# Kernel tuning notes

Hardware: AMD Instinct MI355X
Metric: run time of the kernel (lower is better)

## Reference

```python
import jax, jax.numpy as jnp
import numpy as np
from jax import lax

Tx, Ty, NA, NS = 30, 10, 32, 64
HV, MV = 128, 64
B = 16384


def setup_inputs() -> dict:
    key = jax.random.key(0)
    ks = jax.random.split(key, 16)
    g = lambda k, s: jax.random.normal(k, s, jnp.float32) * 0.05
    return {
        "X": jax.random.normal(ks[0], (B, Tx, HV), jnp.float32),
        # pre-attention bidirectional LSTM (PyTorch gate order i,f,g,o; b = b_ih + b_hh)
        "W_ih_f": g(ks[1], (4 * NA, HV)), "W_hh_f": g(ks[2], (4 * NA, NA)), "b_f": g(ks[3], (4 * NA,)),
        "W_ih_r": g(ks[4], (4 * NA, HV)), "W_hh_r": g(ks[5], (4 * NA, NA)), "b_r": g(ks[6], (4 * NA,)),
        # attention MLP
        "W1": g(ks[7], (10, 2 * NA + NS)), "b1": g(ks[8], (10,)),
        "W2": g(ks[9], (1, 10)), "b2": g(ks[10], (1,)),
        # post-attention LSTM cell
        "W_ih_p": g(ks[11], (4 * NS, 2 * NA)), "W_hh_p": g(ks[12], (4 * NS, NS)), "b_p": g(ks[13], (4 * NS,)),
        # output projection
        "Wo": g(ks[14], (MV, NS)), "bo": g(ks[15], (MV,)),
    }


def _cell(x, h, c, W_ih, W_hh, b):
    # PyTorch LSTM cell, gate order (i, f, g, o)
    z = x @ W_ih.T + h @ W_hh.T + b
    i, f, gg, o = jnp.split(z, 4, axis=-1)
    c = jax.nn.sigmoid(f) * c + jax.nn.sigmoid(i) * jnp.tanh(gg)
    h = jax.nn.sigmoid(o) * jnp.tanh(c)
    return h, c


def _run_lstm(X, W_ih, W_hh, b):
    Bn = X.shape[0]
    H = W_hh.shape[1]
    init = (jnp.zeros((Bn, H), X.dtype), jnp.zeros((Bn, H), X.dtype))

    def step(carry, x_t):
        h, c = _cell(x_t, carry[0], carry[1], W_ih, W_hh, b)
        return (h, c), h

    _, hs = lax.scan(step, init, jnp.swapaxes(X, 0, 1))  # hs: [Tx, B, H]
    return jnp.swapaxes(hs, 0, 1)


def reference(X, W_ih_f, W_hh_f, b_f, W_ih_r, W_hh_r, b_r, W1, b1, W2, b2,
              W_ih_p, W_hh_p, b_p, Wo, bo):
    # bidirectional encoder: a is [B, Tx, 2*NA]
    a_f = _run_lstm(X, W_ih_f, W_hh_f, b_f)
    a_r = _run_lstm(X[:, ::-1, :], W_ih_r, W_hh_r, b_r)[:, ::-1, :]
    a = jnp.concatenate([a_f, a_r], axis=-1)
    Bn = X.shape[0]

    def dec_step(carry, _):
        s, c = carry
        # one_step_attention
        s_rep = jnp.broadcast_to(s[:, None, :], (Bn, Tx, NS))
        cat = jnp.concatenate([a, s_rep], axis=-1)          # [B, Tx, 2*NA+NS]
        e = jnp.tanh(cat @ W1.T + b1)                        # [B, Tx, 10]
        en = jax.nn.relu(e @ W2.T + b2)                      # [B, Tx, 1]
        alphas = jax.nn.softmax(en, axis=1)                  # softmax over Tx
        context = jnp.sum(alphas * a, axis=1)                # [B, 2*NA]
        # post-attention LSTM (single step)
        s, c = _cell(context, s, c, W_ih_p, W_hh_p, b_p)
        out = s @ Wo.T + bo                                  # [B, MV]
        return (s, c), out

    init = (jnp.zeros((Bn, NS), X.dtype), jnp.zeros((Bn, NS), X.dtype))
    _, outs = lax.scan(dec_step, init, None, length=Ty)      # [Ty, B, MV]
    return jnp.swapaxes(outs, 0, 1)                          # [B, Ty, MV]
```

## Files before the change

kernel.cpp:

```cpp
#include <hip/hip_runtime.h>

typedef unsigned short u16;
typedef unsigned int   u32;
typedef __attribute__((ext_vector_type(8))) short short8;
typedef __attribute__((ext_vector_type(4))) float f4;

#define BT 16
#define TX 30
#define TY 10

__device__ __forceinline__ float bf2f_u16(u16 h){ u32 i=((u32)h)<<16; float f; __builtin_memcpy(&f,&i,4); return f; }
__device__ __forceinline__ float lo2f(u32 p){ u32 i=p<<16; float f; __builtin_memcpy(&f,&i,4); return f; }
__device__ __forceinline__ float hi2f(u32 p){ u32 i=p&0xffff0000u; float f; __builtin_memcpy(&f,&i,4); return f; }
__device__ __forceinline__ u16 f2bf(float f){ u32 x; __builtin_memcpy(&x,&f,4); u32 r=(x+0x7fffu+((x>>16)&1u))>>16; return (u16)r; }

#if __has_builtin(__builtin_amdgcn_rcpf)
__device__ __forceinline__ float frcp(float x){ return __builtin_amdgcn_rcpf(x); }
#else
__device__ __forceinline__ float frcp(float x){ return 1.0f/x; }
#endif
__device__ __forceinline__ float sigm(float x){ return frcp(1.0f+__expf(-x)); }
__device__ __forceinline__ float tanh_(float x){ x=fminf(fmaxf(x,-15.0f),15.0f); float e=__expf(2.0f*x); return 1.0f - 2.0f*frcp(e+1.0f); }

__device__ __forceinline__ f4 mfma16(short8 a, short8 b, f4 c){
    return __builtin_amdgcn_mfma_f32_16x16x32_bf16(a, b, c, 0, 0, 0);
}

union S8u { short8 s; u32 u[4]; };

__device__ __forceinline__ void cvt_pair(float a0, float a1, u32& hp, u32& lp){
    u32 u0, u1; __builtin_memcpy(&u0,&a0,4); __builtin_memcpy(&u1,&a1,4);
    hp = __builtin_amdgcn_perm(u1, u0, 0x07060302u);
    float r0 = a0 - hi2f(u0);
    float r1 = a1 - hi2f(u1);
    u32 v0, v1; __builtin_memcpy(&v0,&r0,4); __builtin_memcpy(&v1,&r1,4);
    lp = __builtin_amdgcn_perm(v1, v0, 0x07060302u);
}

struct SDec {
    u16 sh[BT][64], sl[BT][64];
    u16 ctxh[BT][64], ctxl[BT][64];
    float en[BT*TX];
};
struct SEnc {
    u16 h[2][2][2][BT][40];
};
union UU { SEnc e; SDec d; };
struct Smem {
    u16 a[BT*TX][64];
    UU u;
};
static_assert(sizeof(SEnc) == 10240, "enc");
static_assert(sizeof(SDec) == 10112, "dec");
static_assert(sizeof(Smem) == 71680, "LDS 70KB -> 2 blocks/CU");

__global__ __launch_bounds__(256, 2) void fused_kernel(
    const float* __restrict__ X,
    const float* __restrict__ Wihf, const float* __restrict__ Whhf, const float* __restrict__ bfv,
    const float* __restrict__ Wihr, const float* __restrict__ Whhr, const float* __restrict__ brv,
    const float* __restrict__ W1, const float* __restrict__ b1, const float* __restrict__ W2, const float* __restrict__ b2,
    const float* __restrict__ Wihp, const float* __restrict__ Whhp, const float* __restrict__ bp,
    const float* __restrict__ Wo, const float* __restrict__ bo,
    float* __restrict__ out)
{
    __shared__ __align__(16) Smem sm;
    const int tid = threadIdx.x;
    const int b0  = blockIdx.x * BT;

    const int lane = tid & 63;
    const int wv   = tid >> 6;
    const int mL   = lane & 15;
    const int qL   = lane >> 4;
    const int k0q  = qL * 8;
    const int ed   = wv >> 1;
    const int ub   = (wv & 1) * 16;

    {
        u32* p = (u32*)&sm.u.e;
        for (int i = tid; i < 2560; i += 256) p[i] = 0u;
    }
    __syncthreads();

    const float* Wih = ed ? Wihr : Wihf;
    const float* Whh = ed ? Whhr : Whhf;
    const float* bv  = ed ? brv  : bfv;

    short8 Bih[4][4]; short8 Bhh[4]; float bias4[4];
    #pragma unroll
    for (int gt = 0; gt < 4; gt++){
        const int n = gt*32 + ub + mL;
        #pragma unroll
        for (int kt = 0; kt < 4; kt++){
            const float* p = Wih + n*128 + kt*32 + k0q;
            short8 s;
            #pragma unroll
            for (int j = 0; j < 8; j++) s[j] = (short)f2bf(p[j]);
            Bih[gt][kt] = s;
        }
        {
            const float* p = Whh + n*32 + k0q;
            short8 s;
            #pragma unroll
            for (int j = 0; j < 8; j++) s[j] = (short)f2bf(p[j]);
            Bhh[gt] = s;
        }
        bias4[gt] = bv[n];
    }

    const float* xrow = X + ((long)(b0 + mL)) * TX * 128;
    float cst[4] = {0.f,0.f,0.f,0.f};

    auto estep = [&](int t, f4* cur, f4* nxt){
        if (t + 1 < TX){
            const int ts = ed ? (TX-2-t) : (t+1);
            const float* p = xrow + ts*128 + k0q;
            #pragma unroll
            for (int kt = 0; kt < 4; kt++){
                nxt[2*kt]   = *(const f4*)(p + kt*32);
                nxt[2*kt+1] = *(const f4*)(p + kt*32 + 4);
            }
        }
        const int rb = (t+1) & 1, wb = t & 1;

        f4 acc[4];
        #pragma unroll
        for (int gt = 0; gt < 4; gt++) acc[gt] = (f4){bias4[gt],bias4[gt],bias4[gt],bias4[gt]};

        #pragma unroll
        for (int kt = 0; kt < 4; kt++){
            S8u xh, xl;
            cvt_pair(cur[2*kt][0],   cur[2*kt][1],   xh.u[0], xl.u[0]);
            cvt_pair(cur[2*kt][2],   cur[2*kt][3],   xh.u[1], xl.u[1]);
            cvt_pair(cur[2*kt+1][0], cur[2*kt+1][1], xh.u[2], xl.u[2]);
            cvt_pair(cur[2*kt+1][2], cur[2*kt+1][3], xh.u[3], xl.u[3]);
            #pragma unroll
            for (int gt = 0; gt < 4; gt++){
                acc[gt] = mfma16(xh.s, Bih[gt][kt], acc[gt]);
                acc[gt] = mfma16(xl.s, Bih[gt][kt], acc[gt]);
            }
        }
        {
            const short8 Ahh = *(const short8*)&sm.u.e.h[rb][ed][0][mL][k0q];
            const short8 Ahl = *(const short8*)&sm.u.e.h[rb][ed][1][mL][k0q];
            #pragma unroll
            for (int gt = 0; gt < 4; gt++){
                acc[gt] = mfma16(Ahh, Bhh[gt], acc[gt]);
                acc[gt] = mfma16(Ahl, Bhh[gt], acc[gt]);
            }
        }
        const int tpos = ed ? (TX-1-t) : t;
        const int u = ed*32 + ub + mL;
        #pragma unroll
        for (int reg = 0; reg < 4; reg++){
            const int m = qL*4 + reg;
            const float ii = sigm(acc[0][reg]), ff = sigm(acc[1][reg]);
            const float gg = tanh_(acc[2][reg]), oo = sigm(acc[3][reg]);
            cst[reg] = ff*cst[reg] + ii*gg;
            const float hh = oo * tanh_(cst[reg]);
            const u16 hhi = f2bf(hh);
            const u16 hlo = f2bf(hh - bf2f_u16(hhi));
            sm.u.e.h[wb][ed][0][m][ub+mL] = hhi;
            sm.u.e.h[wb][ed][1][m][ub+mL] = hlo;
            const int r = m*TX + tpos;
            sm.a[r][(((u>>3) ^ ((m+tpos)&7))<<3) | (u&7)] = hhi;
        }
        __syncthreads();
    };

    f4 rawA[8], rawB[8];
    {
        const int ts0 = ed ? (TX-1) : 0;
        const float* p = xrow + ts0*128 + k0q;
        #pragma unroll
        for (int kt = 0; kt < 4; kt++){
            rawA[2*kt]   = *(const f4*)(p + kt*32);
            rawA[2*kt+1] = *(const f4*)(p + kt*32 + 4);
        }
    }
    for (int t = 0; t < TX; t += 2){ estep(t, rawA, rawB); estep(t+1, rawB, rawA); }

    {
        u32* z = (u32*)sm.u.d.sh;
        for (int i = tid; i < 1024; i += 256) z[i] = 0u;
    }
    short8 W1aB[2][2];
    #pragma unroll
    for (int kt = 0; kt < 2; kt++){
        short8 hv8, lv8;
        #pragma unroll
        for (int j = 0; j < 8; j++){
            const float v = (mL < 10) ? W1[mL*128 + kt*32 + k0q + j] : 0.f;
            const u16 hb = f2bf(v);
            hv8[j] = (short)hb;
            lv8[j] = (short)f2bf(v - bf2f_u16(hb));
        }
        W1aB[kt][0] = hv8; W1aB[kt][1] = lv8;
    }
    short8 W1sB[2];
    #pragma unroll
    for (int kt = 0; kt < 2; kt++){
        short8 s;
        #pragma unroll
        for (int j = 0; j < 8; j++){
            const float v = (mL < 10) ? W1[mL*128 + 64 + kt*32 + k0q + j] : 0.f;
            s[j] = (short)f2bf(v);
        }
        W1sB[kt] = s;
    }
    const float b1v = (mL < 10) ? b1[mL] : 0.f;
    const float w2v = (mL < 10) ? W2[mL] : 0.f;
    const float b2s = b2[0];

    const int uw = wv * 16;
    short8 Bip[4][2], Bhp[4][2]; float pb4[4];
    #pragma unroll
    for (int gt = 0; gt < 4; gt++){
        const int n = gt*64 + uw + mL;
        #pragma unroll
        for (int kt = 0; kt < 2; kt++){
            const float* p = Wihp + n*64 + kt*32 + k0q;
            const float* q = Whhp + n*64 + kt*32 + k0q;
            short8 s1v, s2v;
            #pragma unroll
            for (int j = 0; j < 8; j++){ s1v[j] = (short)f2bf(p[j]); s2v[j] = (short)f2bf(q[j]); }
            Bip[gt][kt] = s1v; Bhp[gt][kt] = s2v;
        }
        pb4[gt] = bp[n];
    }
    short8 Bo2[2];
    {
        const int n = uw + mL;
        #pragma unroll
        for (int kt = 0; kt < 2; kt++){
            const float* p = Wo + n*64 + kt*32 + k0q;
            short8 s;
            #pragma unroll
            for (int j = 0; j < 8; j++) s[j] = (short)f2bf(p[j]);
            Bo2[kt] = s;
        }
    }
    const float boL = bo[uw + mL];
    float cs2[4] = {0.f,0.f,0.f,0.f};
    const u16* aflat  = &sm.a[0][0];
    u16* shf = &sm.u.d.sh[0][0];
    u16* slf = &sm.u.d.sl[0][0];
    u16* chf = &sm.u.d.ctxh[0][0];
    u16* clf = &sm.u.d.ctxl[0][0];
    __syncthreads();

    for (int ty = 0; ty < TY; ty++){
        for (int tt = wv; tt < TX; tt += 4){
            const int r = tt*16 + mL;
            const int b = (r * 34953) >> 20;
            const int tp2 = r - b*30;
            f4 accE = (f4){b1v, b1v, b1v, b1v};
            const u16* ab = aflat + r*64;
            const int keyA = (b + tp2) & 7;
            #pragma unroll
            for (int kt = 0; kt < 2; kt++){
                const short8 av = *(const short8*)(ab + (((kt*4+qL)^keyA)<<3));
                accE = mfma16(av, W1aB[kt][0], accE);
                accE = mfma16(av, W1aB[kt][1], accE);
            }
            const int keyS = b & 7;
            #pragma unroll
            for (int kt = 0; kt < 2; kt++){
                const int off = b*64 + (((kt*4+qL)^keyS)<<3);
                const short8 shh = *(const short8*)(shf + off);
                const short8 sll = *(const short8*)(slf + off);
                accE = mfma16(shh, W1sB[kt], accE);
                accE = mfma16(sll, W1sB[kt], accE);
            }
            float er[4];
            #pragma unroll
            for (int reg = 0; reg < 4; reg++) er[reg] = w2v * tanh_(accE[reg]);
            #pragma unroll
            for (int d = 1; d < 16; d <<= 1){
                #pragma unroll
                for (int reg = 0; reg < 4; reg++) er[reg] += __shfl_xor(er[reg], d);
            }
            if (mL == 0){
                f4 ev;
                #pragma unroll
                for (int reg = 0; reg < 4; reg++) ev[reg] = fmaxf(er[reg] + b2s, 0.f);
                *(f4*)&sm.u.d.en[tt*16 + qL*4] = ev;
            }
        }
        __syncthreads();
        {
            const int cr = tid >> 4, cup = tid & 15;
            const float* enr = &sm.u.d.en[cr*30];
            float mx = enr[0];
            #pragma unroll
            for (int t2 = 1; t2 < TX; t2++) mx = fmaxf(mx, enr[t2]);
            float ssum = 0.f, s0 = 0.f, s1 = 0.f, s2v_ = 0.f, s3 = 0.f;
            #pragma unroll 5
            for (int t2 = 0; t2 < TX; t2++){
                const float e = __expf(enr[t2]-mx);
                const u16* ap = aflat + (cr*30+t2)*64
                              + ((((cup>>1) ^ ((cr+t2)&7))<<3) | ((cup&1)<<2));
                const u32 pa0 = *(const u32*)ap;
                const u32 pa1 = *(const u32*)(ap + 2);
                ssum += e;
                s0 += e*lo2f(pa0); s1 += e*hi2f(pa0);
                s2v_ += e*lo2f(pa1); s3 += e*hi2f(pa1);
            }
            const float inv = frcp(ssum);
            s0 *= inv; s1 *= inv; s2v_ *= inv; s3 *= inv;
            const u16 h0 = f2bf(s0), h1 = f2bf(s1), h2 = f2bf(s2v_), h3 = f2bf(s3);
            const u16 l0 = f2bf(s0 - bf2f_u16(h0)), l1 = f2bf(s1 - bf2f_u16(h1));
            const u16 l2 = f2bf(s2v_ - bf2f_u16(h2)), l3 = f2bf(s3 - bf2f_u16(h3));
            const int off = cr*64 + ((((cup>>1) ^ (cr&7))<<3) | ((cup&1)<<2));
            *(u32*)(chf + off)     = (u32)h0 | ((u32)h1 << 16);
            *(u32*)(chf + off + 2) = (u32)h2 | ((u32)h3 << 16);
            *(u32*)(clf + off)     = (u32)l0 | ((u32)l1 << 16);
            *(u32*)(clf + off + 2) = (u32)l2 | ((u32)l3 << 16);
        }
        __syncthreads();
        f4 acc2[4];
        #pragma unroll
        for (int gt = 0; gt < 4; gt++) acc2[gt] = (f4){pb4[gt],pb4[gt],pb4[gt],pb4[gt]};
        #pragma unroll
        for (int kt = 0; kt < 2; kt++){
            const int off = mL*64 + (((kt*4+qL) ^ (mL&7))<<3);
            const short8 ch  = *(const short8*)(chf + off);
            const short8 cl  = *(const short8*)(clf + off);
            const short8 shh = *(const short8*)(shf + off);
            const short8 sll = *(const short8*)(slf + off);
            #pragma unroll
            for (int gt = 0; gt < 4; gt++){
                acc2[gt] = mfma16(ch,  Bip[gt][kt], acc2[gt]);
                acc2[gt] = mfma16(cl,  Bip[gt][kt], acc2[gt]);
                acc2[gt] = mfma16(shh, Bhp[gt][kt], acc2[gt]);
                acc2[gt] = mfma16(sll, Bhp[gt][kt], acc2[gt]);
            }
        }
        __syncthreads();
        #pragma unroll
        for (int reg = 0; reg < 4; reg++){
            const int m = qL*4 + reg;
            const float ii = sigm(acc2[0][reg]), ff = sigm(acc2[1][reg]);
            const float gg = tanh_(acc2[2][reg]), oo = sigm(acc2[3][reg]);
            cs2[reg] = ff*cs2[reg] + ii*gg;
            const float sv = oo * tanh_(cs2[reg]);
            const u16 shi = f2bf(sv);
            const u16 slo = f2bf(sv - bf2f_u16(shi));
            const int u2 = uw + mL;
            const int idx = m*64 + ((((u2>>3) ^ (m&7))<<3) | (u2&7));
            shf[idx] = shi;
            slf[idx] = slo;
        }
        __syncthreads();
        f4 acc3 = (f4){boL, boL, boL, boL};
        #pragma unroll
        for (int kt = 0; kt < 2; kt++){
            const int off = mL*64 + (((kt*4+qL) ^ (mL&7))<<3);
            const short8 shh = *(const short8*)(shf + off);
            const short8 sll = *(const short8*)(slf + off);
            acc3 = mfma16(shh, Bo2[kt], acc3);
            acc3 = mfma16(sll, Bo2[kt], acc3);
        }
        #pragma unroll
        for (int reg = 0; reg < 4; reg++){
            const int m = qL*4 + reg;
            out[(((long)(b0+m))*TY + ty)*64 + uw + mL] = acc3[reg];
        }
    }
}

extern "C" void kernel_launch(void* const* d_in, const int* in_sizes, int n_in,
                              void* d_out, int out_size, void* d_ws, size_t ws_size,
                              hipStream_t stream) {
    const float* X    = (const float*)d_in[0];
    const float* Wihf = (const float*)d_in[1];
    const float* Whhf = (const float*)d_in[2];
    const float* bfv  = (const float*)d_in[3];
    const float* Wihr = (const float*)d_in[4];
    const float* Whhr = (const float*)d_in[5];
    const float* brv  = (const float*)d_in[6];
    const float* W1   = (const float*)d_in[7];
    const float* b1   = (const float*)d_in[8];
    const float* W2   = (const float*)d_in[9];
    const float* b2   = (const float*)d_in[10];
    const float* Wihp = (const float*)d_in[11];
    const float* Whhp = (const float*)d_in[12];
    const float* bp   = (const float*)d_in[13];
    const float* Wo   = (const float*)d_in[14];
    const float* bo   = (const float*)d_in[15];
    float* out = (float*)d_out;

    const int B = in_sizes[0] / (TX * 128);
    dim3 grid(B / BT), block(256);
    hipLaunchKernelGGL(fused_kernel, grid, block, 0, stream,
                       X, Wihf, Whhf, bfv, Wihr, Whhr, brv,
                       W1, b1, W2, b2, Wihp, Whhp, bp, Wo, bo, out);
}
```

Baseline: 614.6 us.

## Move encoder outputs to global workspace and precompute decoder-invariant attention term

Adds a templated variant that stores the encoder activations in a global workspace instead of LDS. This cuts LDS per block from 70KB to about 29KB so up to 4 blocks fit per CU. The encoder contribution a·W1ᵀ+b1 is computed once and cached in LDS, so it is no longer recomputed at each of the 10 decoder steps. The cost is that the context reduction now reads the activations from global memory or L2 on every decoder step. If no workspace of sufficient size is provided, the original LDS path is used.

Result: slower. 1.091 ms (+77.5%).

```diff
diff --git a/kernel.cpp b/kernel.cpp
--- a/kernel.cpp
+++ b/kernel.cpp
@@ -37,35 +37,32 @@
     lp = __builtin_amdgcn_perm(v1, v0, 0x07060302u);
 }
 
-struct SDec {
-    u16 sh[BT][64], sl[BT][64];
-    u16 ctxh[BT][64], ctxl[BT][64];
-    float en[BT*TX];
-};
-struct SEnc {
-    u16 h[2][2][2][BT][40];
-};
-union UU { SEnc e; SDec d; };
-struct Smem {
-    u16 a[BT*TX][64];
-    UU u;
-};
-static_assert(sizeof(SEnc) == 10240, "enc");
-static_assert(sizeof(SDec) == 10112, "dec");
-static_assert(sizeof(Smem) == 71680, "LDS 70KB -> 2 blocks/CU");
-
-__global__ __launch_bounds__(256, 2) void fused_kernel(
+struct SEnc  { u16 h[2][2][2][BT][40]; };
+struct SDecL { u16 sh[BT][64], sl[BT][64], ctxh[BT][64], ctxl[BT][64]; float en[BT*TX]; };
+struct SDecG { u16 sh[BT][64], sl[BT][64], ctxh[BT][64], ctxl[BT][64]; float en[BT*TX]; float aW1[BT*TX*10]; };
+template<bool AG> struct SmemT;
+template<> struct SmemT<false> { u16 a[BT*TX][64]; union { SEnc e; SDecL d; } u; };
+template<> struct SmemT<true>  { union { SEnc e; SDecG d; } u; };
+static_assert(sizeof(SmemT<false>) == 71680, "fallback LDS");
+static_assert(sizeof(SmemT<true>)  == 29312, "global-a LDS");
+
+template<bool AG>
+__global__ __launch_bounds__(256, AG ? 4 : 2) void fused_kernel(
     const float* __restrict__ X,
     const float* __restrict__ Wihf, const float* __restrict__ Whhf, const float* __restrict__ bfv,
     const float* __restrict__ Wihr, const float* __restrict__ Whhr, const float* __restrict__ brv,
     const float* __restrict__ W1, const float* __restrict__ b1, const float* __restrict__ W2, const float* __restrict__ b2,
     const float* __restrict__ Wihp, const float* __restrict__ Whhp, const float* __restrict__ bp,
     const float* __restrict__ Wo, const float* __restrict__ bo,
+    u16* __restrict__ aws,
     float* __restrict__ out)
 {
-    __shared__ __align__(16) Smem sm;
+    __shared__ __align__(16) SmemT<AG> sm;
     const int tid = threadIdx.x;
     const int b0  = blockIdx.x * BT;
+
+    u16* awb = nullptr;
+    if constexpr (AG) awb = aws + (size_t)blockIdx.x * (BT*TX*64);
 
     const int lane = tid & 63;
     const int wv   = tid >> 6;
@@ -162,7 +159,8 @@
             sm.u.e.h[wb][ed][0][m][ub+mL] = hhi;
             sm.u.e.h[wb][ed][1][m][ub+mL] = hlo;
             const int r = m*TX + tpos;
-            sm.a[r][(((u>>3) ^ ((m+tpos)&7))<<3) | (u&7)] = hhi;
+            if constexpr (AG) awb[r*64 + u] = hhi;
+            else sm.a[r][(((u>>3) ^ ((m+tpos)&7))<<3) | (u&7)] = hhi;
         }
         __syncthreads();
     };
@@ -183,6 +181,9 @@
         u32* z = (u32*)sm.u.d.sh;
         for (int i = tid; i < 1024; i += 256) z[i] = 0u;
     }
+    const u16* aflat;
+    if constexpr (AG) aflat = awb; else aflat = &sm.a[0][0];
+
     short8 W1aB[2][2];
     #pragma unroll
     for (int kt = 0; kt < 2; kt++){
@@ -211,6 +212,24 @@
     const float w2v = (mL < 10) ? W2[mL] : 0.f;
     const float b2s = b2[0];
 
+    if constexpr (AG){
+        for (int tile = wv; tile < 30; tile += 4){
+            f4 accA = (f4){b1v, b1v, b1v, b1v};
+            const u16* ab = aflat + (tile*16 + mL)*64;
+            #pragma unroll
+            for (int kt = 0; kt < 2; kt++){
+                const short8 av = *(const short8*)(ab + kt*32 + k0q);
+                accA = mfma16(av, W1aB[kt][0], accA);
+                accA = mfma16(av, W1aB[kt][1], accA);
+            }
+            if (mL < 10){
+                #pragma unroll
+                for (int reg = 0; reg < 4; reg++)
+                    sm.u.d.aW1[(tile*16 + qL*4 + reg)*10 + mL] = accA[reg];
+            }
+        }
+    }
+
     const int uw = wv * 16;
     short8 Bip[4][2], Bhp[4][2]; float pb4[4];
     #pragma unroll
@@ -241,7 +260,6 @@
     }
     const float boL = bo[uw + mL];
     float cs2[4] = {0.f,0.f,0.f,0.f};
-    const u16* aflat  = &sm.a[0][0];
     u16* shf = &sm.u.d.sh[0][0];
     u16* slf = &sm.u.d.sl[0][0];
     u16* chf = &sm.u.d.ctxh[0][0];
@@ -253,14 +271,21 @@
             const int r = tt*16 + mL;
             const int b = (r * 34953) >> 20;
             const int tp2 = r - b*30;
-            f4 accE = (f4){b1v, b1v, b1v, b1v};
-            const u16* ab = aflat + r*64;
-            const int keyA = (b + tp2) & 7;
-            #pragma unroll
-            for (int kt = 0; kt < 2; kt++){
-                const short8 av = *(const short8*)(ab + (((kt*4+qL)^keyA)<<3));
-                accE = mfma16(av, W1aB[kt][0], accE);
-                accE = mfma16(av, W1aB[kt][1], accE);
+            f4 accE;
+            if constexpr (AG){
+                #pragma unroll
+                for (int reg = 0; reg < 4; reg++)
+                    accE[reg] = (mL < 10) ? sm.u.d.aW1[(tt*16 + qL*4 + reg)*10 + mL] : 0.f;
+            } else {
+                accE = (f4){b1v, b1v, b1v, b1v};
+                const u16* ab = aflat + r*64;
+                const int keyA = (b + tp2) & 7;
+                #pragma unroll
+                for (int kt = 0; kt < 2; kt++){
+                    const short8 av = *(const short8*)(ab + (((kt*4+qL)^keyA)<<3));
+                    accE = mfma16(av, W1aB[kt][0], accE);
+                    accE = mfma16(av, W1aB[kt][1], accE);
+                }
             }
             const int keyS = b & 7;
             #pragma unroll
@@ -297,7 +322,9 @@
             #pragma unroll 5
             for (int t2 = 0; t2 < TX; t2++){
                 const float e = __expf(enr[t2]-mx);
-                const u16* ap = aflat + (cr*30+t2)*64
+                const u16* ap;
+                if constexpr (AG) ap = aflat + (cr*30+t2)*64 + (cup<<2);
+                else ap = aflat + (cr*30+t2)*64
                               + ((((cup>>1) ^ ((cr+t2)&7))<<3) | ((cup&1)<<2));
                 const u32 pa0 = *(const u32*)ap;
                 const u32 pa1 = *(const u32*)(ap + 2);
@@ -389,9 +416,17 @@
     const float* bo   = (const float*)d_in[15];
     float* out = (float*)d_out;
 
-    const int B = in_sizes[0] / (TX * 128);
-    dim3 grid(B / BT), block(256);
-    hipLaunchKernelGGL(fused_kernel, grid, block, 0, stream,
-                       X, Wihf, Whhf, bfv, Wihr, Whhr, brv,
-                       W1, b1, W2, b2, Wihp, Whhp, bp, Wo, bo, out);
+    const int B  = in_sizes[0] / (TX * 128);
+    const int nb = B / BT;
+    dim3 grid(nb), block(256);
+    const size_t need = (size_t)nb * (BT*TX*64) * sizeof(u16);
+    if (d_ws != nullptr && ws_size >= need){
+        fused_kernel<true><<<grid, block, 0, stream>>>(
+            X, Wihf, Whhf, bfv, Wihr, Whhr, brv,
+            W1, b1, W2, b2, Wihp, Whhp, bp, Wo, bo, (u16*)d_ws, out);
+    } else {
+        fused_kernel<false><<<grid, block, 0, stream>>>(
+            X, Wihf, Whhf, bfv, Wihr, Whhr, brv,
+            W1, b1, W2, b2, Wihp, Whhp, bp, Wo, bo, nullptr, out);
+    }
 }
```
